# Kernel tuning notes

Hardware: AMD Instinct MI355X
Metric: run time of the kernel (lower is better)

## Reference

```python
import jax, jax.numpy as jnp
import numpy as np

# ---- static module config (matches init_kwargs) ----
N = 16384
E_DIM = 256
SHARE_N_E = 2048
SPECIFIC = [1024, 1024, 1024]
TOTAL_N_E = SHARE_N_E + sum(SPECIFIC)  # 5120
BETA = 0.25
NUM_MOD = len(SPECIFIC)
BIG = 1e7  # value written into masked-out distance entries

# prefix boundaries of the per-modality code blocks: [2048, 3072, 4096, 5120]
CODE_BOUNDS = jnp.asarray(np.cumsum([SHARE_N_E] + SPECIFIC)[:, None].squeeze(-1) if False else np.cumsum([SHARE_N_E] + SPECIFIC), dtype=jnp.int32)
# code -> modality id; shared codes get -1
CODE_MOD = jnp.searchsorted(CODE_BOUNDS, jnp.arange(TOTAL_N_E, dtype=jnp.int32), side='right') - 1  # [TOTAL_N_E]


def setup_inputs() -> dict:
    key = jax.random.key(0)
    k1, k2 = jax.random.split(key)
    x = jax.random.normal(k1, (N, E_DIM), dtype=jnp.float32)
    emb_weight = jax.random.normal(k2, (TOTAL_N_E, E_DIM), dtype=jnp.float32)  # nn.Embedding default N(0,1)
    split_index = jnp.array([0, 5120, 10240, 16384], dtype=jnp.int64)  # 3 equal modality segments
    return {"x": x, "emb_weight": emb_weight, "split_index": split_index}


def reference(x, emb_weight, split_index):
    # pairwise squared distances d[n, c] = ||x_n||^2 + ||e_c||^2 - 2 x_n . e_c
    d = (jnp.sum(x * x, axis=1, keepdims=True)
         + jnp.sum(emb_weight * emb_weight, axis=1)[None, :]
         - 2.0 * jnp.einsum('nd,cd->nc', x, emb_weight))  # [N, TOTAL_N_E]

    # token -> modality id via split boundaries (vectorized form of the Python loop)
    tok_mod = jnp.searchsorted(split_index, jnp.arange(N, dtype=split_index.dtype), side='right') - 1  # [N]
    tok_mod = tok_mod.astype(jnp.int32)
    # allowed = shared code OR code's modality matches token's modality
    allowed = (CODE_MOD[None, :] == -1) | (CODE_MOD[None, :] == tok_mod[:, None])  # [N, TOTAL_N_E]
    d = jnp.where(allowed, d, jnp.float32(BIG))

    indices = jnp.argmin(d, axis=-1)              # [N]
    x_q = jnp.take(emb_weight, indices, axis=0)   # [N, E_DIM]

    # per-modality VQ losses: codebook + beta * commitment (mse over segment)
    sg = jax.lax.stop_gradient
    se_commit = jnp.sum((sg(x_q) - x) ** 2, axis=1)   # [N]
    se_code = jnp.sum((x_q - sg(x)) ** 2, axis=1)     # [N]
    seg_commit = jax.ops.segment_sum(se_commit, tok_mod, num_segments=NUM_MOD)
    seg_code = jax.ops.segment_sum(se_code, tok_mod, num_segments=NUM_MOD)
    counts = (split_index[1:] - split_index[:-1]).astype(jnp.float32) * jnp.float32(E_DIM)
    q_losses = seg_code / counts + BETA * (seg_commit / counts)  # [NUM_MOD]

    # straight-through estimator
    x_q_ste = x + sg(x_q - x)
    return (x_q_ste, indices, d, q_losses)
```

## Files before the change

### kernel.cpp

```cpp
#include <hip/hip_runtime.h>
#include <stdint.h>

#define N_TOK    16384
#define E_DIM    256
#define N_CODE   5120
#define N_SHARED 2048
#define BIGF     1e7f

#define BM  128
#define BN  128
#define BK  32
#define NCB (N_CODE / BN)
#define NKC (E_DIM / BK)
#define CHUNK (BM * BK)

#define IDX_OFF ((size_t)N_TOK * E_DIM)
#define D_OFF   (IDX_OFF + N_TOK)
#define QL_OFF  (D_OFF + (size_t)N_TOK * N_CODE)

typedef float f32x4 __attribute__((ext_vector_type(4)));
typedef short bf16x8 __attribute__((ext_vector_type(8)));
typedef short s16x4 __attribute__((ext_vector_type(4)));

typedef __attribute__((address_space(1))) const unsigned int g_u32;
typedef __attribute__((address_space(3))) unsigned int lds_u32;

__device__ __forceinline__ unsigned short bf16_rn(float f) {
    unsigned u = __float_as_uint(f);
    u += 0x7FFF + ((u >> 16) & 1);
    return (unsigned short)(u >> 16);
}
__device__ __forceinline__ float bf16_to_f(unsigned short h) {
    return __uint_as_float(((unsigned)h) << 16);
}

__global__ __launch_bounds__(256) void convert_kernel(const float* __restrict__ x,
                                                      const float* __restrict__ emb,
                                                      float* __restrict__ xx,
                                                      float* __restrict__ ee,
                                                      short* __restrict__ xhi, short* __restrict__ xlo,
                                                      short* __restrict__ ehi, short* __restrict__ elo) {
    int wid = threadIdx.x >> 6, ln = threadIdx.x & 63;
    int row = blockIdx.x * 4 + wid;
    const float* src; float* nrm; short *hiA, *loA; int rl, tb;
    if (row < N_TOK) {
        src = x + (size_t)row * E_DIM; nrm = xx + row;
        tb = row >> 7; rl = row & 127; hiA = xhi; loA = xlo;
    } else {
        int r = row - N_TOK;
        src = emb + (size_t)r * E_DIM; nrm = ee + r;
        tb = r >> 7; rl = r & 127; hiA = ehi; loA = elo;
    }
    f32x4 v = ((const f32x4*)src)[ln];
    float s = v[0]*v[0] + v[1]*v[1] + v[2]*v[2] + v[3]*v[3];
    s16x4 h, l;
#pragma unroll
    for (int c = 0; c < 4; ++c) {
        unsigned short hh = bf16_rn(v[c]);
        h[c] = (short)hh;
        l[c] = (short)bf16_rn(v[c] - bf16_to_f(hh));
    }
    int kc = ln >> 3, q = (ln >> 1) & 3, kl4 = (ln & 1) * 4;
    size_t di = ((((size_t)tb * NKC + kc) * 4 + q) * BM + rl) * 8 + kl4;
    *(s16x4*)&hiA[di] = h;
    *(s16x4*)&loA[di] = l;
#pragma unroll
    for (int sh = 32; sh; sh >>= 1) s += __shfl_xor(s, sh, 64);
    if (ln == 0) *nrm = s;
}

__global__ __launch_bounds__(256, 2) void gemm_kernel(const short* __restrict__ xhi,
                                                      const short* __restrict__ xlo,
                                                      const short* __restrict__ ehi,
                                                      const short* __restrict__ elo,
                                                      const int* __restrict__ split,
                                                      const float* __restrict__ xx,
                                                      const float* __restrict__ ee,
                                                      float* __restrict__ out) {
    __shared__ short Ah[CHUNK], Al[CHUNK], Bh[CHUNK], Bl[CHUNK];
    __shared__ float xxs[BM];
    __shared__ float ees[BN];
    __shared__ float redv[2][BM];
    __shared__ int   redi[2][BM];

    const int bx = blockIdx.x;
    const int by = blockIdx.y;
    const int m0 = by * BM, n0 = bx * BN;
    const int t = threadIdx.x;

    const int s1 = split[1], s2v = split[2];
    const int tmFirst = (m0 >= s1) + (m0 >= s2v);
    const int tmLast  = ((m0 + BM - 1) >= s1) + ((m0 + BM - 1) >= s2v);
    const bool rowUni = (tmFirst == tmLast);
    const int cmod = (n0 < N_SHARED) ? -1 : ((n0 - N_SHARED) >> 10);

    float* dOut = out + D_OFF;
    float* pmin = out;
    int*   pidx = (int*)(out + (size_t)N_TOK * NCB);

    if (cmod >= 0 && rowUni && cmod != tmFirst) {
        int row = t >> 1, ch = t & 1;
        f32x4* p = (f32x4*)(dOut + (size_t)(m0 + row) * N_CODE + n0 + ch * 64);
        f32x4 big = {BIGF, BIGF, BIGF, BIGF};
#pragma unroll
        for (int u = 0; u < 16; ++u) p[u] = big;
        if (t < BM) {
            pmin[(size_t)(m0 + t) * NCB + bx] = BIGF;
            pidx[(size_t)(m0 + t) * NCB + bx] = n0;
        }
        return;
    }

    const bool allAllowed = (cmod < 0) || (rowUni && cmod == tmFirst);

    if (t < BM) xxs[t] = xx[m0 + t];
    else        ees[t - BM] = ee[n0 + (t - BM)];

    f32x4 acc[4][4] = {};

    const int wid = t >> 6, lane = t & 63;
    const int quad = lane >> 4, ln16 = lane & 15;
    const int wr = (wid >> 1) * 64, wc = (wid & 1) * 64;

    const short* aHiG = xhi + (size_t)by * NKC * CHUNK;
    const short* aLoG = xlo + (size_t)by * NKC * CHUNK;
    const short* bHiG = ehi + (size_t)bx * NKC * CHUNK;
    const short* bLoG = elo + (size_t)bx * NKC * CHUNK;
    const int tOff = t * 8;

    for (int kc = 0; kc < NKC; ++kc) {
        __syncthreads();
        const int co = kc * CHUNK;
#pragma unroll
        for (int p = 0; p < 2; ++p) {
            int o = p * 2048 + tOff;
            __builtin_amdgcn_global_load_lds((g_u32*)(aHiG + co + o), (lds_u32*)&Ah[o], 16, 0, 0);
            __builtin_amdgcn_global_load_lds((g_u32*)(aLoG + co + o), (lds_u32*)&Al[o], 16, 0, 0);
            __builtin_amdgcn_global_load_lds((g_u32*)(bHiG + co + o), (lds_u32*)&Bh[o], 16, 0, 0);
            __builtin_amdgcn_global_load_lds((g_u32*)(bLoG + co + o), (lds_u32*)&Bl[o], 16, 0, 0);
        }
        __syncthreads();

        bf16x8 ah[4], al[4], bh[4], bl[4];
#pragma unroll
        for (int i = 0; i < 4; ++i) {
            int a = (quad * BM + wr + i * 16 + ln16) * 8;
            ah[i] = *(const bf16x8*)&Ah[a];
            al[i] = *(const bf16x8*)&Al[a];
        }
#pragma unroll
        for (int j = 0; j < 4; ++j) {
            int b = (quad * BM + wc + j * 16 + ln16) * 8;
            bh[j] = *(const bf16x8*)&Bh[b];
            bl[j] = *(const bf16x8*)&Bl[b];
        }
#pragma unroll
        for (int i = 0; i < 4; ++i)
#pragma unroll
            for (int j = 0; j < 4; ++j) {
                acc[i][j] = __builtin_amdgcn_mfma_f32_16x16x32_bf16(ah[i], bh[j], acc[i][j], 0, 0, 0);
                acc[i][j] = __builtin_amdgcn_mfma_f32_16x16x32_bf16(ah[i], bl[j], acc[i][j], 0, 0, 0);
                acc[i][j] = __builtin_amdgcn_mfma_f32_16x16x32_bf16(al[i], bh[j], acc[i][j], 0, 0, 0);
            }
    }

#pragma unroll
    for (int i = 0; i < 4; ++i) {
#pragma unroll
        for (int r = 0; r < 4; ++r) {
            int lm = wr + i * 16 + quad * 4 + r;
            int gm = m0 + lm;
            float xv = xxs[lm];
            int tmod = (gm >= s1) + (gm >= s2v);
            float best = 3.4e38f;
            int bidx = n0;
#pragma unroll
            for (int j = 0; j < 4; ++j) {
                int lnn = wc + j * 16 + ln16;
                int gn = n0 + lnn;
                float dv = fmaf(-2.f, acc[i][j][r], xv + ees[lnn]);
                if (!allAllowed) {
                    bool ok = (gn < N_SHARED) || (((gn - N_SHARED) >> 10) == tmod);
                    if (!ok) dv = BIGF;
                }
                dOut[(size_t)gm * N_CODE + gn] = dv;
                if (dv < best) { best = dv; bidx = gn; }
            }
#pragma unroll
            for (int s = 1; s < 16; s <<= 1) {
                float ov = __shfl_xor(best, s, 64);
                int   oi = __shfl_xor(bidx, s, 64);
                if (ov < best || (ov == best && oi < bidx)) { best = ov; bidx = oi; }
            }
            if (ln16 == 0) { redv[wid & 1][lm] = best; redi[wid & 1][lm] = bidx; }
        }
    }
    __syncthreads();
    if (t < BM) {
        float v0 = redv[0][t]; int i0 = redi[0][t];
        float v1 = redv[1][t]; int i1 = redi[1][t];
        if (v1 < v0 || (v1 == v0 && i1 < i0)) { v0 = v1; i0 = i1; }
        pmin[(size_t)(m0 + t) * NCB + bx] = v0;
        pidx[(size_t)(m0 + t) * NCB + bx] = i0;
    }
}

__global__ __launch_bounds__(256) void reduce_kernel(float* __restrict__ out) {
    int tk = blockIdx.x * 256 + threadIdx.x;
    const float* pmin = out;
    const int* pidx = (const int*)(out + (size_t)N_TOK * NCB);
    float best = pmin[(size_t)tk * NCB];
    int bi = pidx[(size_t)tk * NCB];
    for (int j = 1; j < NCB; ++j) {
        float v = pmin[(size_t)tk * NCB + j];
        int ii = pidx[(size_t)tk * NCB + j];
        if (v < best || (v == best && ii < bi)) { best = v; bi = ii; }
    }
    out[IDX_OFF + tk] = (float)bi;
}

__global__ __launch_bounds__(256) void gather_kernel(const float* __restrict__ x,
                                                     const float* __restrict__ emb,
                                                     const int* __restrict__ split,
                                                     float* __restrict__ out,
                                                     float* __restrict__ wsLoss) {
    __shared__ float ls[3];
    int t = threadIdx.x, wid = t >> 6, ln = t & 63;
    if (t < 3) ls[t] = 0.f;
    __syncthreads();
    int tok = blockIdx.x * 4 + wid;
    int idx = (int)out[IDX_OFF + tok];
    f32x4 e  = ((const f32x4*)(emb + (size_t)idx * E_DIM))[ln];
    f32x4 xv = ((const f32x4*)(x + (size_t)tok * E_DIM))[ln];
    f32x4 q;
    float s = 0.f;
#pragma unroll
    for (int c = 0; c < 4; ++c) {
        float d = e[c] - xv[c];
        q[c] = xv[c] + d;
        s = fmaf(d, d, s);
    }
    ((f32x4*)(out + (size_t)tok * E_DIM))[ln] = q;
#pragma unroll
    for (int sh = 32; sh; sh >>= 1) s += __shfl_xor(s, sh, 64);
    if (ln == 0) {
        int mod = (tok >= split[1]) + (tok >= split[2]);
        atomicAdd(&ls[mod], s);
    }
    __syncthreads();
    if (t < 3) wsLoss[blockIdx.x * 3 + t] = ls[t];
}

__global__ __launch_bounds__(256) void loss_kernel(const float* __restrict__ wsLoss,
                                                   const int* __restrict__ split,
                                                   float* __restrict__ out, int nblk) {
    __shared__ float red[256];
    float s[3] = {0.f, 0.f, 0.f};
    for (int b = threadIdx.x; b < nblk; b += 256) {
        s[0] += wsLoss[b * 3 + 0];
        s[1] += wsLoss[b * 3 + 1];
        s[2] += wsLoss[b * 3 + 2];
    }
    for (int m = 0; m < 3; ++m) {
        red[threadIdx.x] = s[m];
        __syncthreads();
        for (int st = 128; st; st >>= 1) {
            if (threadIdx.x < st) red[threadIdx.x] += red[threadIdx.x + st];
            __syncthreads();
        }
        if (threadIdx.x == 0) {
            float cnt = (float)(split[m + 1] - split[m]) * (float)E_DIM;
            float a = red[0] / cnt;
            out[QL_OFF + m] = a + 0.25f * a;
        }
        __syncthreads();
    }
}

extern "C" void kernel_launch(void* const* d_in, const int* in_sizes, int n_in,
                              void* d_out, int out_size, void* d_ws, size_t ws_size,
                              hipStream_t stream) {
    const float* x   = (const float*)d_in[0];
    const float* emb = (const float*)d_in[1];
    const int* split = (const int*)d_in[2];
    float* out = (float*)d_out;

    float* xx     = (float*)d_ws;
    float* ee     = xx + N_TOK;
    float* wsLoss = ee + N_CODE;
    short* xhi    = (short*)(wsLoss + 4096 * 3);
    short* xlo    = xhi + (size_t)N_TOK * E_DIM;
    short* ehi    = xlo + (size_t)N_TOK * E_DIM;
    short* elo    = ehi + (size_t)N_CODE * E_DIM;
    int nblkGather = N_TOK / 4;

    convert_kernel<<<dim3((N_TOK + N_CODE) / 4), dim3(256), 0, stream>>>(x, emb, xx, ee, xhi, xlo, ehi, elo);
    gemm_kernel<<<dim3(NCB, N_TOK / BM), dim3(256), 0, stream>>>(xhi, xlo, ehi, elo, split, xx, ee, out);
    reduce_kernel<<<dim3(N_TOK / 256), dim3(256), 0, stream>>>(out);
    gather_kernel<<<dim3(nblkGather), dim3(256), 0, stream>>>(x, emb, split, out, wsLoss);
    loss_kernel<<<dim3(1), dim3(256), 0, stream>>>(wsLoss, split, out, nblkGather);
}
```

Measured before the change: 488.2 us.

## Fuse argmin reduction into gather, remap grid by XCD, use nontemporal stores

Removes the separate reduce kernel: gather now reads the 40 per-tile partial minima with one wave per token and reduces them with shuffles. The GEMM grid becomes 1D and is remapped so each XCD handles a contiguous group of 5 code columns, which should improve L2 reuse of codebook tiles. The large distance matrix and x_q outputs are written with nontemporal stores to avoid polluting cache, and the partial buffers move from the output buffer to the workspace. The gain is mostly one fewer launch and better cache behaviour, at the cost of more workspace use.

New measurement: 715.0 us. +46.5%, slower.

```diff
diff --git a/kernel.cpp b/kernel.cpp
--- a/kernel.cpp
+++ b/kernel.cpp
@@ -76,6 +76,8 @@
                                                       const int* __restrict__ split,
                                                       const float* __restrict__ xx,
                                                       const float* __restrict__ ee,
+                                                      float* __restrict__ pmin,
+                                                      int* __restrict__ pidx,
                                                       float* __restrict__ out) {
     __shared__ short Ah[CHUNK], Al[CHUNK], Bh[CHUNK], Bl[CHUNK];
     __shared__ float xxs[BM];
@@ -83,8 +85,11 @@
     __shared__ float redv[2][BM];
     __shared__ int   redi[2][BM];
 
-    const int bx = blockIdx.x;
-    const int by = blockIdx.y;
+    const int g = blockIdx.x;
+    const int xcd = g & 7;
+    const int s = g >> 3;
+    const int by = s / 5;
+    const int bx = xcd * 5 + (s - by * 5);
     const int m0 = by * BM, n0 = bx * BN;
     const int t = threadIdx.x;
 
@@ -95,15 +100,13 @@
     const int cmod = (n0 < N_SHARED) ? -1 : ((n0 - N_SHARED) >> 10);
 
     float* dOut = out + D_OFF;
-    float* pmin = out;
-    int*   pidx = (int*)(out + (size_t)N_TOK * NCB);
 
     if (cmod >= 0 && rowUni && cmod != tmFirst) {
         int row = t >> 1, ch = t & 1;
         f32x4* p = (f32x4*)(dOut + (size_t)(m0 + row) * N_CODE + n0 + ch * 64);
         f32x4 big = {BIGF, BIGF, BIGF, BIGF};
 #pragma unroll
-        for (int u = 0; u < 16; ++u) p[u] = big;
+        for (int u = 0; u < 16; ++u) __builtin_nontemporal_store(big, p + u);
         if (t < BM) {
             pmin[(size_t)(m0 + t) * NCB + bx] = BIGF;
             pidx[(size_t)(m0 + t) * NCB + bx] = n0;
@@ -183,13 +186,13 @@
                     bool ok = (gn < N_SHARED) || (((gn - N_SHARED) >> 10) == tmod);
                     if (!ok) dv = BIGF;
                 }
-                dOut[(size_t)gm * N_CODE + gn] = dv;
+                __builtin_nontemporal_store(dv, &dOut[(size_t)gm * N_CODE + gn]);
                 if (dv < best) { best = dv; bidx = gn; }
             }
 #pragma unroll
-            for (int s = 1; s < 16; s <<= 1) {
-                float ov = __shfl_xor(best, s, 64);
-                int   oi = __shfl_xor(bidx, s, 64);
+            for (int sh = 1; sh < 16; sh <<= 1) {
+                float ov = __shfl_xor(best, sh, 64);
+                int   oi = __shfl_xor(bidx, sh, 64);
                 if (ov < best || (ov == best && oi < bidx)) { best = ov; bidx = oi; }
             }
             if (ln16 == 0) { redv[wid & 1][lm] = best; redi[wid & 1][lm] = bidx; }
@@ -205,23 +208,11 @@
     }
 }
 
-__global__ __launch_bounds__(256) void reduce_kernel(float* __restrict__ out) {
-    int tk = blockIdx.x * 256 + threadIdx.x;
-    const float* pmin = out;
-    const int* pidx = (const int*)(out + (size_t)N_TOK * NCB);
-    float best = pmin[(size_t)tk * NCB];
-    int bi = pidx[(size_t)tk * NCB];
-    for (int j = 1; j < NCB; ++j) {
-        float v = pmin[(size_t)tk * NCB + j];
-        int ii = pidx[(size_t)tk * NCB + j];
-        if (v < best || (v == best && ii < bi)) { best = v; bi = ii; }
-    }
-    out[IDX_OFF + tk] = (float)bi;
-}
-
 __global__ __launch_bounds__(256) void gather_kernel(const float* __restrict__ x,
                                                      const float* __restrict__ emb,
                                                      const int* __restrict__ split,
+                                                     const float* __restrict__ pmin,
+                                                     const int* __restrict__ pidx,
                                                      float* __restrict__ out,
                                                      float* __restrict__ wsLoss) {
     __shared__ float ls[3];
@@ -229,8 +220,22 @@
     if (t < 3) ls[t] = 0.f;
     __syncthreads();
     int tok = blockIdx.x * 4 + wid;
-    int idx = (int)out[IDX_OFF + tok];
-    f32x4 e  = ((const f32x4*)(emb + (size_t)idx * E_DIM))[ln];
+
+    float best = 3.4e38f;
+    int bi = 0x7fffffff;
+    if (ln < NCB) {
+        best = pmin[(size_t)tok * NCB + ln];
+        bi   = pidx[(size_t)tok * NCB + ln];
+    }
+#pragma unroll
+    for (int sh = 1; sh < 64; sh <<= 1) {
+        float ov = __shfl_xor(best, sh, 64);
+        int   oi = __shfl_xor(bi, sh, 64);
+        if (ov < best || (ov == best && oi < bi)) { best = ov; bi = oi; }
+    }
+    if (ln == 0) out[IDX_OFF + tok] = (float)bi;
+
+    f32x4 e  = ((const f32x4*)(emb + (size_t)bi * E_DIM))[ln];
     f32x4 xv = ((const f32x4*)(x + (size_t)tok * E_DIM))[ln];
     f32x4 q;
     float s = 0.f;
@@ -240,7 +245,7 @@
         q[c] = xv[c] + d;
         s = fmaf(d, d, s);
     }
-    ((f32x4*)(out + (size_t)tok * E_DIM))[ln] = q;
+    __builtin_nontemporal_store(q, &((f32x4*)(out + (size_t)tok * E_DIM))[ln]);
 #pragma unroll
     for (int sh = 32; sh; sh >>= 1) s += __shfl_xor(s, sh, 64);
     if (ln == 0) {
@@ -288,15 +293,16 @@
     float* xx     = (float*)d_ws;
     float* ee     = xx + N_TOK;
     float* wsLoss = ee + N_CODE;
-    short* xhi    = (short*)(wsLoss + 4096 * 3);
+    float* pmin   = wsLoss + 4096 * 3;
+    int*   pidx   = (int*)(pmin + (size_t)N_TOK * NCB);
+    short* xhi    = (short*)(pidx + (size_t)N_TOK * NCB);
     short* xlo    = xhi + (size_t)N_TOK * E_DIM;
     short* ehi    = xlo + (size_t)N_TOK * E_DIM;
     short* elo    = ehi + (size_t)N_CODE * E_DIM;
     int nblkGather = N_TOK / 4;
 
     convert_kernel<<<dim3((N_TOK + N_CODE) / 4), dim3(256), 0, stream>>>(x, emb, xx, ee, xhi, xlo, ehi, elo);
-    gemm_kernel<<<dim3(NCB, N_TOK / BM), dim3(256), 0, stream>>>(xhi, xlo, ehi, elo, split, xx, ee, out);
-    reduce_kernel<<<dim3(N_TOK / 256), dim3(256), 0, stream>>>(out);
-    gather_kernel<<<dim3(nblkGather), dim3(256), 0, stream>>>(x, emb, split, out, wsLoss);
+    gemm_kernel<<<dim3(NCB * (N_TOK / BM)), dim3(256), 0, stream>>>(xhi, xlo, ehi, elo, split, xx, ee, pmin, pidx, out);
+    gather_kernel<<<dim3(nblkGather), dim3(256), 0, stream>>>(x, emb, split, pmin, pidx, out, wsLoss);
     loss_kernel<<<dim3(1), dim3(256), 0, stream>>>(wsLoss, split, out, nblkGather);
 }
```
